# Optimization experiments

Hardware: AMD Instinct MI355X
Metric: run time of the kernel (lower is better)

## Reference

```python
import jax, jax.numpy as jnp
import numpy as np


def _side(x, y, W, w):
    # x: [B, Lx, d] attends over y: [B, Ly, d]
    alpha = jnp.einsum('bld,de->ble', x, W)          # bilinear projection
    alpha = jnp.einsum('ble,bme->blm', alpha, y)     # [B, Lx, Ly]
    alpha = jax.nn.softmax(alpha, axis=1)            # Keras softmax axis=1 (over Lx)
    a = jnp.einsum('blm,bmd->bld', alpha, y)         # attended context [B, Lx, d]
    out = jnp.concatenate([x - a, x * a], axis=-1)   # [B, Lx, 2d]
    beta = jax.nn.softmax(jnp.einsum('ble,eo->blo', out, w)[..., 0], axis=-1)  # [B, Lx]
    return jnp.einsum('bl,ble->be', beta, out)       # pooled [B, 2d]


def setup_inputs() -> dict:
    key = jax.random.key(0)
    k1, k2, k3, k4 = jax.random.split(key, 4)
    B, L, d = 512, 256, 512
    return {
        'i': jax.random.normal(k1, (B, L, d), dtype=jnp.float32),
        'j': jax.random.normal(k2, (B, L, d), dtype=jnp.float32),
        'W': jax.random.normal(k3, (d, d), dtype=jnp.float32) * 0.05,
        'w': jax.random.normal(k4, (2 * d, 1), dtype=jnp.float32) * 0.05,
    }


def reference(i, j, W, w):
    out_i = _side(i, j, W, w)
    out_j = _side(j, i, W, w)
    return (out_i, out_j)
```

## Files before the change

kernel.cpp:

```cpp
#include <hip/hip_runtime.h>

#define LL 256
#define DD 512

typedef _Float16 f16;
typedef _Float16 f16x4_t __attribute__((ext_vector_type(4)));
typedef _Float16 f16x8_t __attribute__((ext_vector_type(8)));
typedef float f32x4_t __attribute__((ext_vector_type(4)));

__device__ __forceinline__ f16x8_t cvt2(const float4 a, const float4 b) {
  f16x8_t v;
  v[0] = (f16)a.x; v[1] = (f16)a.y; v[2] = (f16)a.z; v[3] = (f16)a.w;
  v[4] = (f16)b.x; v[5] = (f16)b.y; v[6] = (f16)b.z; v[7] = (f16)b.w;
  return v;
}

__device__ __forceinline__ void gl16(const void* g, void* l) {
  __builtin_amdgcn_global_load_lds(
      (const __attribute__((address_space(1))) void*)g,
      (__attribute__((address_space(3))) void*)l, 16, 0, 0);
}

__global__ void k_prep(const float* __restrict__ W, f16* __restrict__ Wt) {
  __shared__ float t[64][65];
  int bx = blockIdx.x & 7;
  int by = blockIdx.x >> 3;
  int tx = threadIdx.x & 63, tg = threadIdx.x >> 6;
  for (int r = tg; r < 64; r += 4)
    t[r][tx] = W[(by * 64 + r) * DD + bx * 64 + tx];
  __syncthreads();
  for (int r = tg; r < 64; r += 4)
    Wt[(bx * 64 + r) * DD + by * 64 + tx] = (f16)t[tx][r];
}


__global__ __launch_bounds__(512, 2)
void k_main(const float* __restrict__ gi, const float* __restrict__ gj,
            const f16* __restrict__ Wt, const float* __restrict__ wv,
            f16* __restrict__ slabs, float* __restrict__ out) {
  __shared__ __align__(16) char R1[131072];
  __shared__ __align__(16) char R2[16384];

  const int tid = threadIdx.x;
  const int lane = tid & 63;
  const int wave = tid >> 6;
  const int lq = lane & 15, lg = lane >> 4;

  const int sb = blockIdx.x;
  const int wk = (sb & 7) * 128 + (sb >> 3);
  const int b = wk >> 1, side = wk & 1;
  const float* __restrict__ x = (side ? gj : gi) + (size_t)b * (LL * DD);
  const float* __restrict__ y = (side ? gi : gj) + (size_t)b * (LL * DD);
  f16* __restrict__ slab = slabs + (size_t)wk * (LL * DD);

  char* const R1c = R1;
  char* const R2c = R2;
  float* const colred = (float*)R2c;
  float* const colmax = (float*)(R2c + 2048);
  float* const colinv = (float*)(R2c + 3072);
  float* const gp     = (float*)R2c;
  float* const betas  = (float*)(R2c + 2048);

  {
    const int wl2 = wave & 1, we4 = wave >> 1;
    for (int lh = 0; lh < 2; ++lh) {
      f32x4_t acc[4][8];
#pragma unroll
      for (int lf = 0; lf < 4; ++lf)
#pragma unroll
        for (int ef = 0; ef < 8; ++ef) acc[lf][ef] = (f32x4_t){0.f, 0.f, 0.f, 0.f};

      const int xrow = tid >> 2;
      const int xc4 = (tid & 3) * 16;
      {
        const float* src = x + (size_t)(lh * 128 + xrow) * DD + xc4;
        float4 a0 = *(const float4*)src, a1 = *(const float4*)(src + 4);
        float4 a2 = *(const float4*)(src + 8), a3 = *(const float4*)(src + 12);
        unsigned swz = (unsigned)(xrow & 7) << 4;
        *(f16x8_t*)(R1c + xrow * 128 + ((xc4 * 2) ^ swz)) = cvt2(a0, a1);
        *(f16x8_t*)(R1c + xrow * 128 + ((xc4 * 2 + 16) ^ swz)) = cvt2(a2, a3);
      }
      __syncthreads();

      for (int s = 0; s < 8; ++s) {
        char* xbc = R1c + (s & 1) * 16384;
        char* xbn = R1c + ((s + 1) & 1) * 16384;
        float4 p0, p1, p2, p3;
        if (s < 7) {
          const float* src = x + (size_t)(lh * 128 + xrow) * DD + (s + 1) * 64 + xc4;
          p0 = *(const float4*)src; p1 = *(const float4*)(src + 4);
          p2 = *(const float4*)(src + 8); p3 = *(const float4*)(src + 12);
        }
#pragma unroll
        for (int ks = 0; ks < 2; ++ks) {
          f16x8_t aF[4], bF[8];
#pragma unroll
          for (int lf = 0; lf < 4; ++lf) {
            int row = wl2 * 64 + lf * 16 + lq;
            aF[lf] = *(const f16x8_t*)(xbc + row * 128 +
                       ((ks * 64 + lg * 16) ^ ((unsigned)(row & 7) << 4)));
          }
#pragma unroll
          for (int ef = 0; ef < 8; ++ef) {
            int er = we4 * 128 + ef * 16 + lq;
            bF[ef] = *(const f16x8_t*)(Wt + (size_t)er * DD + s * 64 + ks * 32 + lg * 8);
          }
#pragma unroll
          for (int lf = 0; lf < 4; ++lf)
#pragma unroll
            for (int ef = 0; ef < 8; ++ef)
              acc[lf][ef] = __builtin_amdgcn_mfma_f32_16x16x32_f16(aF[lf], bF[ef], acc[lf][ef], 0, 0, 0);
        }
        if (s < 7) {
          unsigned swz = (unsigned)(xrow & 7) << 4;
          *(f16x8_t*)(xbn + xrow * 128 + ((xc4 * 2) ^ swz)) = cvt2(p0, p1);
          *(f16x8_t*)(xbn + xrow * 128 + ((xc4 * 2 + 16) ^ swz)) = cvt2(p2, p3);
        }
        __syncthreads();
      }
#pragma unroll
      for (int lf = 0; lf < 4; ++lf)
#pragma unroll
        for (int ef = 0; ef < 8; ++ef) {
          int e = we4 * 128 + ef * 16 + lq;
          int l0 = lh * 128 + wl2 * 64 + lf * 16 + lg * 4;
#pragma unroll
          for (int r = 0; r < 4; ++r) {
            int l = l0 + r;
            size_t byte = (size_t)l * 1024 + (size_t)(e >> 6) * 128 +
                          (unsigned)(((e & 63) * 2) ^ ((l & 7) << 4));
            *(f16*)((char*)slab + byte) = (f16)acc[lf][ef][r];
          }
        }
    }
  }
  __threadfence_block();
  __syncthreads();

  {
    const int wm = wave & 3, wl = wave >> 2;
    f32x4_t accS[4][8];
#pragma unroll
    for (int mf = 0; mf < 4; ++mf)
#pragma unroll
      for (int nf = 0; nf < 8; ++nf) accS[mf][nf] = (f32x4_t){0.f, 0.f, 0.f, 0.f};

    const int prow = tid >> 1, phalf = tid & 1;
    const int lsub = lane >> 3, lin8 = lane & 7;

    auto stageBP = [&](int s, int buf) {
#pragma unroll
      for (int q = 0; q < 4; ++q) {
        int lrow = (q * 8 + wave) * 8 + lsub;
        const char* g = (const char*)slab + (size_t)lrow * 1024 + (size_t)s * 128 + lin8 * 16;
        gl16(g, R1c + buf * 32768 + (q * 8 + wave) * 1024);
      }
    };

    stageBP(0, 0);
    {
      unsigned swz = (unsigned)(prow & 7) << 4;
      const float* src = y + (size_t)prow * DD + phalf * 32;
#pragma unroll
      for (int q = 0; q < 4; ++q) {
        float4 a0 = *(const float4*)(src + q * 8);
        float4 a1 = *(const float4*)(src + q * 8 + 4);
        *(f16x8_t*)(R1c + 65536 + prow * 128 + ((phalf * 64 + q * 16) ^ swz)) = cvt2(a0, a1);
      }
    }
    __syncthreads();

    for (int s = 0; s < 8; ++s) {
      const char* BPc = R1c + (s & 1) * 32768;
      const char* Yc = R1c + 65536 + (s & 1) * 32768;
      float4 pre_y[8];
      if (s < 7) {
        stageBP(s + 1, (s + 1) & 1);
        const float* src = y + (size_t)prow * DD + (s + 1) * 64 + phalf * 32;
#pragma unroll
        for (int q = 0; q < 8; ++q) pre_y[q] = *(const float4*)(src + q * 4);
      }
#pragma unroll
      for (int ks = 0; ks < 2; ++ks) {
        f16x8_t aF[4], bF[8];
#pragma unroll
        for (int mf = 0; mf < 4; ++mf) {
          int row = wm * 64 + mf * 16 + lq;
          aF[mf] = *(const f16x8_t*)(Yc + row * 128 +
                     ((ks * 64 + lg * 16) ^ ((unsigned)(row & 7) << 4)));
        }
#pragma unroll
        for (int nf = 0; nf < 8; ++nf) {
          int row = wl * 128 + nf * 16 + lq;
          bF[nf] = *(const f16x8_t*)(BPc + row * 128 +
                     ((ks * 64 + lg * 16) ^ ((unsigned)(row & 7) << 4)));
        }
#pragma unroll
        for (int mf = 0; mf < 4; ++mf)
#pragma unroll
          for (int nf = 0; nf < 8; ++nf)
            accS[mf][nf] = __builtin_amdgcn_mfma_f32_16x16x32_f16(aF[mf], bF[nf], accS[mf][nf], 0, 0, 0);
      }
      if (s < 7) {
        char* Yn = R1c + 65536 + ((s + 1) & 1) * 32768;
        unsigned swz = (unsigned)(prow & 7) << 4;
#pragma unroll
        for (int q = 0; q < 4; ++q)
          *(f16x8_t*)(Yn + prow * 128 + ((phalf * 64 + q * 16) ^ swz)) =
              cvt2(pre_y[2 * q], pre_y[2 * q + 1]);
      }
      __syncthreads();
    }

    float red[4][4];
#pragma unroll
    for (int mf = 0; mf < 4; ++mf)
#pragma unroll
      for (int r = 0; r < 4; ++r) {
        float v = accS[mf][0][r];
#pragma unroll
        for (int nf = 1; nf < 8; ++nf) v = fmaxf(v, accS[mf][nf][r]);
        v = fmaxf(v, __shfl_xor(v, 1));
        v = fmaxf(v, __shfl_xor(v, 2));
        v = fmaxf(v, __shfl_xor(v, 4));
        v = fmaxf(v, __shfl_xor(v, 8));
        red[mf][r] = v;
      }
    if (lq == 0) {
#pragma unroll
      for (int mf = 0; mf < 4; ++mf)
#pragma unroll
        for (int r = 0; r < 4; ++r)
          colred[wl * 256 + wm * 64 + mf * 16 + lg * 4 + r] = red[mf][r];
    }
    __syncthreads();
    if (tid < 256) colmax[tid] = fmaxf(colred[tid], colred[256 + tid]);
    __syncthreads();
    float cm[4][4];
#pragma unroll
    for (int mf = 0; mf < 4; ++mf)
#pragma unroll
      for (int r = 0; r < 4; ++r) cm[mf][r] = colmax[wm * 64 + mf * 16 + lg * 4 + r];
    __syncthreads();
#pragma unroll
    for (int mf = 0; mf < 4; ++mf)
#pragma unroll
      for (int r = 0; r < 4; ++r) {
        float s = 0.f;
#pragma unroll
        for (int nf = 0; nf < 8; ++nf) {
          float p = __expf(accS[mf][nf][r] - cm[mf][r]);
          accS[mf][nf][r] = p;
          s += p;
        }
        s += __shfl_xor(s, 1);
        s += __shfl_xor(s, 2);
        s += __shfl_xor(s, 4);
        s += __shfl_xor(s, 8);
        red[mf][r] = s;
      }
    if (lq == 0) {
#pragma unroll
      for (int mf = 0; mf < 4; ++mf)
#pragma unroll
        for (int r = 0; r < 4; ++r)
          colred[wl * 256 + wm * 64 + mf * 16 + lg * 4 + r] = red[mf][r];
    }
    __syncthreads();
    if (tid < 256) colinv[tid] = 1.f / (colred[tid] + colred[256 + tid]);
    __syncthreads();
    float inv[4][4];
#pragma unroll
    for (int mf = 0; mf < 4; ++mf)
#pragma unroll
      for (int r = 0; r < 4; ++r) inv[mf][r] = colinv[wm * 64 + mf * 16 + lg * 4 + r];
    __syncthreads();
#pragma unroll
    for (int mf = 0; mf < 4; ++mf)
#pragma unroll
      for (int nf = 0; nf < 8; ++nf) {
        int l = wl * 128 + nf * 16 + lq;
        f16x4_t v;
        v[0] = (f16)(accS[mf][nf][0] * inv[mf][0]);
        v[1] = (f16)(accS[mf][nf][1] * inv[mf][1]);
        v[2] = (f16)(accS[mf][nf][2] * inv[mf][2]);
        v[3] = (f16)(accS[mf][nf][3] * inv[mf][3]);
        *(f16x4_t*)(R1c + l * 512 +
                    ((wm * 128 + mf * 32 + lg * 8) ^ ((unsigned)(l & 7) << 4))) = v;
      }
  }
  __syncthreads();

  {
    const int wl3 = wave & 3, wd = wave >> 2;
    float garr[4][4];
#pragma unroll
    for (int lf = 0; lf < 4; ++lf)
#pragma unroll
      for (int r = 0; r < 4; ++r) garr[lf][r] = 0.f;

    const int yd = tid & 127, ymq = tid >> 7;
    f16* const a_ = slab;

    for (int dct = 0; dct < 4; ++dct) {
      f32x4_t accB[4][4];
#pragma unroll
      for (int lf = 0; lf < 4; ++lf)
#pragma unroll
        for (int df = 0; df < 4; ++df) accB[lf][df] = (f32x4_t){0.f, 0.f, 0.f, 0.f};

      float lyA[4][4], lyB[4][4];
#pragma unroll
      for (int q = 0; q < 4; ++q) {
        int m0 = ymq * 16 + q * 4;
#pragma unroll
        for (int k = 0; k < 4; ++k)
          lyA[q][k] = y[(size_t)(m0 + k) * DD + dct * 128 + yd];
      }
#pragma unroll
      for (int mh = 0; mh < 4; ++mh) {
        __syncthreads();
        {
          unsigned swz = (unsigned)(yd & 7) << 4;
#pragma unroll
          for (int q = 0; q < 4; ++q) {
            int m0 = ymq * 16 + q * 4;
            f16x4_t v;
            if (mh & 1) {
              v[0] = (f16)lyB[q][0]; v[1] = (f16)lyB[q][1];
              v[2] = (f16)lyB[q][2]; v[3] = (f16)lyB[q][3];
            } else {
              v[0] = (f16)lyA[q][0]; v[1] = (f16)lyA[q][1];
              v[2] = (f16)lyA[q][2]; v[3] = (f16)lyA[q][3];
            }
            *(f16x4_t*)(R2c + yd * 128 + ((m0 * 2) ^ swz)) = v;
          }
        }
        __syncthreads();
        if (mh < 3) {
#pragma unroll
          for (int q = 0; q < 4; ++q) {
            int m0 = (mh + 1) * 64 + ymq * 16 + q * 4;
#pragma unroll
            for (int k = 0; k < 4; ++k) {
              float lv = y[(size_t)(m0 + k) * DD + dct * 128 + yd];
              if (mh & 1) lyA[q][k] = lv; else lyB[q][k] = lv;
            }
          }
        }
#pragma unroll
        for (int ks = 0; ks < 2; ++ks) {
          f16x8_t aF[4], bF[4];
#pragma unroll
          for (int lf = 0; lf < 4; ++lf) {
            int row = wl3 * 64 + lf * 16 + lq;
            aF[lf] = *(const f16x8_t*)(R1c + row * 512 +
                       ((mh * 128 + ks * 64 + lg * 16) ^ ((unsigned)(row & 7) << 4)));
          }
#pragma unroll
          for (int df = 0; df < 4; ++df) {
            int row = wd * 64 + df * 16 + lq;
            bF[df] = *(const f16x8_t*)(R2c + row * 128 +
                       ((ks * 64 + lg * 16) ^ ((unsigned)(row & 7) << 4)));
          }
#pragma unroll
          for (int lf = 0; lf < 4; ++lf)
#pragma unroll
            for (int df = 0; df < 4; ++df)
              accB[lf][df] = __builtin_amdgcn_mfma_f32_16x16x32_f16(aF[lf], bF[df], accB[lf][df], 0, 0, 0);
        }
      }
      float wvA[4], wvB[4];
#pragma unroll
      for (int df = 0; df < 4; ++df) {
        int d = dct * 128 + wd * 64 + df * 16 + lq;
        wvA[df] = wv[d];
        wvB[df] = wv[DD + d];
      }
#pragma unroll
      for (int lf = 0; lf < 4; ++lf)
#pragma unroll
        for (int r = 0; r < 4; ++r) {
          int l = wl3 * 64 + lf * 16 + lg * 4 + r;
          float gs = 0.f;
#pragma unroll
          for (int df = 0; df < 4; ++df) {
            int d = dct * 128 + wd * 64 + df * 16 + lq;
            float av = accB[lf][df][r];
            float xv = x[(size_t)l * DD + d];
            gs += (xv - av) * wvA[df] + (xv * av) * wvB[df];
            a_[(size_t)l * DD + d] = (f16)av;
          }
          gs += __shfl_xor(gs, 1);
          gs += __shfl_xor(gs, 2);
          gs += __shfl_xor(gs, 4);
          gs += __shfl_xor(gs, 8);
          garr[lf][r] += gs;
        }
    }
    __syncthreads();
    if (lq == 0) {
#pragma unroll
      for (int lf = 0; lf < 4; ++lf)
#pragma unroll
        for (int r = 0; r < 4; ++r)
          gp[wd * 256 + wl3 * 64 + lf * 16 + lg * 4 + r] = garr[lf][r];
    }
  }
  __threadfence_block();
  __syncthreads();

  if (wave == 0) {
    float gv[4];
    float M = -3.4e38f;
#pragma unroll
    for (int q = 0; q < 4; ++q) {
      int l = lane + q * 64;
      gv[q] = gp[l] + gp[256 + l];
      M = fmaxf(M, gv[q]);
    }
#pragma unroll
    for (int s = 1; s < 64; s <<= 1) M = fmaxf(M, __shfl_xor(M, s));
    float S = 0.f, ev[4];
#pragma unroll
    for (int q = 0; q < 4; ++q) { ev[q] = __expf(gv[q] - M); S += ev[q]; }
#pragma unroll
    for (int s = 1; s < 64; s <<= 1) S += __shfl_xor(S, s);
    float inv = 1.f / S;
#pragma unroll
    for (int q = 0; q < 4; ++q) betas[lane + q * 64] = ev[q] * inv;
  }
  __syncthreads();

  {
    const f16* const a_ = slab;
    int dc = tid;
    float s1 = 0.f, s2 = 0.f;
    for (int l = 0; l < 256; ++l) {
      float bl = betas[l];
      float av = (float)a_[(size_t)l * DD + dc];
      float xv = x[(size_t)l * DD + dc];
      s1 += bl * (xv - av);
      s2 += bl * (xv * av);
    }
    size_t o = (size_t)side * (512u * 1024u) + (size_t)b * 1024u;
    out[o + dc] = s1;
    out[o + DD + dc] = s2;
  }
}

extern "C" void kernel_launch(void* const* d_in, const int* in_sizes, int n_in,
                              void* d_out, int out_size, void* d_ws, size_t ws_size,
                              hipStream_t stream) {
  (void)in_sizes; (void)n_in; (void)out_size; (void)ws_size;
  const float* gi = (const float*)d_in[0];
  const float* gj = (const float*)d_in[1];
  const float* W  = (const float*)d_in[2];
  const float* wv = (const float*)d_in[3];
  float* out = (float*)d_out;
  f16* Wt = (f16*)d_ws;
  f16* slabs = Wt + DD * DD;
  k_prep<<<dim3(64), dim3(256), 0, stream>>>(W, Wt);
  k_main<<<dim3(1024), dim3(512), 0, stream>>>(gi, gj, Wt, wv, slabs, out);
}
```

Baseline: 959.5 us.

## Fuse projection into score GEMM, keeping projected tiles in LDS instead of global slab

```diff
diff --git a/kernel.cpp b/kernel.cpp
--- a/kernel.cpp
+++ b/kernel.cpp
@@ -13,12 +13,6 @@
   v[0] = (f16)a.x; v[1] = (f16)a.y; v[2] = (f16)a.z; v[3] = (f16)a.w;
   v[4] = (f16)b.x; v[5] = (f16)b.y; v[6] = (f16)b.z; v[7] = (f16)b.w;
   return v;
-}
-
-__device__ __forceinline__ void gl16(const void* g, void* l) {
-  __builtin_amdgcn_global_load_lds(
-      (const __attribute__((address_space(1))) void*)g,
-      (__attribute__((address_space(3))) void*)l, 16, 0, 0);
 }
 
 __global__ void k_prep(const float* __restrict__ W, f16* __restrict__ Wt) {
@@ -55,242 +49,182 @@
 
   char* const R1c = R1;
   char* const R2c = R2;
-  float* const colred = (float*)R2c;
-  float* const colmax = (float*)(R2c + 2048);
-  float* const colinv = (float*)(R2c + 3072);
-  float* const gp     = (float*)R2c;
-  float* const betas  = (float*)(R2c + 2048);
-
-  {
-    const int wl2 = wave & 1, we4 = wave >> 1;
-    for (int lh = 0; lh < 2; ++lh) {
-      f32x4_t acc[4][8];
-#pragma unroll
-      for (int lf = 0; lf < 4; ++lf)
-#pragma unroll
-        for (int ef = 0; ef < 8; ++ef) acc[lf][ef] = (f32x4_t){0.f, 0.f, 0.f, 0.f};
-
-      const int xrow = tid >> 2;
-      const int xc4 = (tid & 3) * 16;
+
+  f32x4_t accS[2][16];
+#pragma unroll
+  for (int mf = 0; mf < 2; ++mf)
+#pragma unroll
+    for (int nfg = 0; nfg < 16; ++nfg) accS[mf][nfg] = (f32x4_t){0.f, 0.f, 0.f, 0.f};
+
+  const int wvl = wave & 1, wve = wave >> 1;
+  const int xrow = tid >> 3, xsl = tid & 7;
+  const int prow = tid >> 1, phalf = tid & 1;
+
+#pragma unroll
+  for (int q = 0; q < 4; ++q) {
+#pragma unroll
+    for (int eh = 0; eh < 2; ++eh) {
+      f32x4_t acc[4][2];
+#pragma unroll
+      for (int ef = 0; ef < 4; ++ef)
+#pragma unroll
+        for (int lf = 0; lf < 2; ++lf) acc[ef][lf] = (f32x4_t){0.f, 0.f, 0.f, 0.f};
+
       {
-        const float* src = x + (size_t)(lh * 128 + xrow) * DD + xc4;
+        const float* src = x + (size_t)(q * 64 + xrow) * DD + xsl * 8;
         float4 a0 = *(const float4*)src, a1 = *(const float4*)(src + 4);
-        float4 a2 = *(const float4*)(src + 8), a3 = *(const float4*)(src + 12);
-        unsigned swz = (unsigned)(xrow & 7) << 4;
-        *(f16x8_t*)(R1c + xrow * 128 + ((xc4 * 2) ^ swz)) = cvt2(a0, a1);
-        *(f16x8_t*)(R1c + xrow * 128 + ((xc4 * 2 + 16) ^ swz)) = cvt2(a2, a3);
+        *(f16x8_t*)(R2c + xrow * 128 + ((xsl * 16) ^ ((unsigned)(xrow & 7) << 4))) =
+            cvt2(a0, a1);
       }
       __syncthreads();
 
       for (int s = 0; s < 8; ++s) {
-        char* xbc = R1c + (s & 1) * 16384;
-        char* xbn = R1c + ((s + 1) & 1) * 16384;
-        float4 p0, p1, p2, p3;
+        char* xc = R2c + (s & 1) * 8192;
+        char* xn = R2c + ((s + 1) & 1) * 8192;
+        float4 p0, p1;
         if (s < 7) {
-          const float* src = x + (size_t)(lh * 128 + xrow) * DD + (s + 1) * 64 + xc4;
+          const float* src = x + (size_t)(q * 64 + xrow) * DD + (s + 1) * 64 + xsl * 8;
           p0 = *(const float4*)src; p1 = *(const float4*)(src + 4);
-          p2 = *(const float4*)(src + 8); p3 = *(const float4*)(src + 12);
         }
 #pragma unroll
         for (int ks = 0; ks < 2; ++ks) {
-          f16x8_t aF[4], bF[8];
-#pragma unroll
-          for (int lf = 0; lf < 4; ++lf) {
-            int row = wl2 * 64 + lf * 16 + lq;
-            aF[lf] = *(const f16x8_t*)(xbc + row * 128 +
-                       ((ks * 64 + lg * 16) ^ ((unsigned)(row & 7) << 4)));
-          }
-#pragma unroll
-          for (int ef = 0; ef < 8; ++ef) {
-            int er = we4 * 128 + ef * 16 + lq;
-            bF[ef] = *(const f16x8_t*)(Wt + (size_t)er * DD + s * 64 + ks * 32 + lg * 8);
-          }
-#pragma unroll
-          for (int lf = 0; lf < 4; ++lf)
-#pragma unroll
-            for (int ef = 0; ef < 8; ++ef)
-              acc[lf][ef] = __builtin_amdgcn_mfma_f32_16x16x32_f16(aF[lf], bF[ef], acc[lf][ef], 0, 0, 0);
+          f16x8_t aF[4], bF[2];
+#pragma unroll
+          for (int ef = 0; ef < 4; ++ef) {
+            int e = eh * 256 + wve * 64 + ef * 16 + lq;
+            aF[ef] = *(const f16x8_t*)(Wt + (size_t)e * DD + s * 64 + ks * 32 + lg * 8);
+          }
+#pragma unroll
+          for (int lf = 0; lf < 2; ++lf) {
+            int l = wvl * 32 + lf * 16 + lq;
+            bF[lf] = *(const f16x8_t*)(xc + l * 128 +
+                       ((ks * 64 + lg * 16) ^ ((unsigned)(l & 7) << 4)));
+          }
+#pragma unroll
+          for (int ef = 0; ef < 4; ++ef)
+#pragma unroll
+            for (int lf = 0; lf < 2; ++lf)
+              acc[ef][lf] = __builtin_amdgcn_mfma_f32_16x16x32_f16(aF[ef], bF[lf], acc[ef][lf], 0, 0, 0);
         }
         if (s < 7) {
-          unsigned swz = (unsigned)(xrow & 7) << 4;
-          *(f16x8_t*)(xbn + xrow * 128 + ((xc4 * 2) ^ swz)) = cvt2(p0, p1);
-          *(f16x8_t*)(xbn + xrow * 128 + ((xc4 * 2 + 16) ^ swz)) = cvt2(p2, p3);
+          *(f16x8_t*)(xn + xrow * 128 + ((xsl * 16) ^ ((unsigned)(xrow & 7) << 4))) =
+              cvt2(p0, p1);
         }
         __syncthreads();
       }
 #pragma unroll
-      for (int lf = 0; lf < 4; ++lf)
-#pragma unroll
-        for (int ef = 0; ef < 8; ++ef) {
-          int e = we4 * 128 + ef * 16 + lq;
-          int l0 = lh * 128 + wl2 * 64 + lf * 16 + lg * 4;
-#pragma unroll
-          for (int r = 0; r < 4; ++r) {
-            int l = l0 + r;
-            size_t byte = (size_t)l * 1024 + (size_t)(e >> 6) * 128 +
-                          (unsigned)(((e & 63) * 2) ^ ((l & 7) << 4));
-            *(f16*)((char*)slab + byte) = (f16)acc[lf][ef][r];
-          }
-        }
-    }
-  }
-  __threadfence_block();
-  __syncthreads();
-
-  {
-    const int wm = wave & 3, wl = wave >> 2;
-    f32x4_t accS[4][8];
-#pragma unroll
-    for (int mf = 0; mf < 4; ++mf)
-#pragma unroll
-      for (int nf = 0; nf < 8; ++nf) accS[mf][nf] = (f32x4_t){0.f, 0.f, 0.f, 0.f};
-
-    const int prow = tid >> 1, phalf = tid & 1;
-    const int lsub = lane >> 3, lin8 = lane & 7;
-
-    auto stageBP = [&](int s, int buf) {
-#pragma unroll
-      for (int q = 0; q < 4; ++q) {
-        int lrow = (q * 8 + wave) * 8 + lsub;
-        const char* g = (const char*)slab + (size_t)lrow * 1024 + (size_t)s * 128 + lin8 * 16;
-        gl16(g, R1c + buf * 32768 + (q * 8 + wave) * 1024);
-      }
-    };
-
-    stageBP(0, 0);
+      for (int ef = 0; ef < 4; ++ef)
+#pragma unroll
+        for (int lf = 0; lf < 2; ++lf) {
+          int l_loc = wvl * 32 + lf * 16 + lq;
+          int e0 = eh * 256 + wve * 64 + ef * 16 + lg * 4;
+          f16x4_t v;
+          v[0] = (f16)acc[ef][lf][0]; v[1] = (f16)acc[ef][lf][1];
+          v[2] = (f16)acc[ef][lf][2]; v[3] = (f16)acc[ef][lf][3];
+          *(f16x4_t*)(R1c + l_loc * 1024 + (e0 >> 6) * 128 +
+                      (((unsigned)((e0 & 63) * 2)) ^ ((unsigned)(l_loc & 7) << 4))) = v;
+        }
+    }
+    __syncthreads();
+
     {
-      unsigned swz = (unsigned)(prow & 7) << 4;
       const float* src = y + (size_t)prow * DD + phalf * 32;
-#pragma unroll
-      for (int q = 0; q < 4; ++q) {
-        float4 a0 = *(const float4*)(src + q * 8);
-        float4 a1 = *(const float4*)(src + q * 8 + 4);
-        *(f16x8_t*)(R1c + 65536 + prow * 128 + ((phalf * 64 + q * 16) ^ swz)) = cvt2(a0, a1);
+      unsigned bk = (unsigned)(prow & 7) << 4;
+#pragma unroll
+      for (int u = 0; u < 4; ++u) {
+        float4 a0 = *(const float4*)(src + u * 8);
+        float4 a1 = *(const float4*)(src + u * 8 + 4);
+        *(f16x8_t*)(R1c + 65536 + prow * 128 + ((phalf * 64 + u * 16) ^ bk)) = cvt2(a0, a1);
       }
     }
     __syncthreads();
 
     for (int s = 0; s < 8; ++s) {
-      const char* BPc = R1c + (s & 1) * 32768;
       const char* Yc = R1c + 65536 + (s & 1) * 32768;
       float4 pre_y[8];
       if (s < 7) {
-        stageBP(s + 1, (s + 1) & 1);
         const float* src = y + (size_t)prow * DD + (s + 1) * 64 + phalf * 32;
 #pragma unroll
-        for (int q = 0; q < 8; ++q) pre_y[q] = *(const float4*)(src + q * 4);
+        for (int u = 0; u < 8; ++u) pre_y[u] = *(const float4*)(src + u * 4);
       }
 #pragma unroll
       for (int ks = 0; ks < 2; ++ks) {
-        f16x8_t aF[4], bF[8];
-#pragma unroll
-        for (int mf = 0; mf < 4; ++mf) {
-          int row = wm * 64 + mf * 16 + lq;
-          aF[mf] = *(const f16x8_t*)(Yc + row * 128 +
-                     ((ks * 64 + lg * 16) ^ ((unsigned)(row & 7) << 4)));
-        }
-#pragma unroll
-        for (int nf = 0; nf < 8; ++nf) {
-          int row = wl * 128 + nf * 16 + lq;
-          bF[nf] = *(const f16x8_t*)(BPc + row * 128 +
-                     ((ks * 64 + lg * 16) ^ ((unsigned)(row & 7) << 4)));
-        }
-#pragma unroll
-        for (int mf = 0; mf < 4; ++mf)
-#pragma unroll
-          for (int nf = 0; nf < 8; ++nf)
-            accS[mf][nf] = __builtin_amdgcn_mfma_f32_16x16x32_f16(aF[mf], bF[nf], accS[mf][nf], 0, 0, 0);
+        f16x8_t aF[2], bF[4];
+#pragma unroll
+        for (int mf = 0; mf < 2; ++mf) {
+          int m = wave * 32 + mf * 16 + lq;
+          aF[mf] = *(const f16x8_t*)(Yc + m * 128 +
+                     ((ks * 64 + lg * 16) ^ ((unsigned)(m & 7) << 4)));
+        }
+#pragma unroll
+        for (int nf = 0; nf < 4; ++nf) {
+          int l_loc = nf * 16 + lq;
+          bF[nf] = *(const f16x8_t*)(R1c + l_loc * 1024 + s * 128 +
+                     ((ks * 64 + lg * 16) ^ ((unsigned)(l_loc & 7) << 4)));
+        }
+#pragma unroll
+        for (int mf = 0; mf < 2; ++mf)
+#pragma unroll
+          for (int nf = 0; nf < 4; ++nf)
+            accS[mf][q * 4 + nf] =
+                __builtin_amdgcn_mfma_f32_16x16x32_f16(aF[mf], bF[nf], accS[mf][q * 4 + nf], 0, 0, 0);
       }
       if (s < 7) {
         char* Yn = R1c + 65536 + ((s + 1) & 1) * 32768;
-        unsigned swz = (unsigned)(prow & 7) << 4;
-#pragma unroll
-        for (int q = 0; q < 4; ++q)
-          *(f16x8_t*)(Yn + prow * 128 + ((phalf * 64 + q * 16) ^ swz)) =
-              cvt2(pre_y[2 * q], pre_y[2 * q + 1]);
+        unsigned bk = (unsigned)(prow & 7) << 4;
+#pragma unroll
+        for (int u = 0; u < 4; ++u)
+          *(f16x8_t*)(Yn + prow * 128 + ((phalf * 64 + u * 16) ^ bk)) =
+              cvt2(pre_y[2 * u], pre_y[2 * u + 1]);
       }
       __syncthreads();
     }
-
-    float red[4][4];
-#pragma unroll
-    for (int mf = 0; mf < 4; ++mf)
-#pragma unroll
-      for (int r = 0; r < 4; ++r) {
-        float v = accS[mf][0][r];
-#pragma unroll
-        for (int nf = 1; nf < 8; ++nf) v = fmaxf(v, accS[mf][nf][r]);
-        v = fmaxf(v, __shfl_xor(v, 1));
-        v = fmaxf(v, __shfl_xor(v, 2));
-        v = fmaxf(v, __shfl_xor(v, 4));
-        v = fmaxf(v, __shfl_xor(v, 8));
-        red[mf][r] = v;
-      }
-    if (lq == 0) {
-#pragma unroll
-      for (int mf = 0; mf < 4; ++mf)
-#pragma unroll
-        for (int r = 0; r < 4; ++r)
-          colred[wl * 256 + wm * 64 + mf * 16 + lg * 4 + r] = red[mf][r];
-    }
-    __syncthreads();
-    if (tid < 256) colmax[tid] = fmaxf(colred[tid], colred[256 + tid]);
-    __syncthreads();
-    float cm[4][4];
-#pragma unroll
-    for (int mf = 0; mf < 4; ++mf)
-#pragma unroll
-      for (int r = 0; r < 4; ++r) cm[mf][r] = colmax[wm * 64 + mf * 16 + lg * 4 + r];
-    __syncthreads();
-#pragma unroll
-    for (int mf = 0; mf < 4; ++mf)
-#pragma unroll
-      for (int r = 0; r < 4; ++r) {
-        float s = 0.f;
-#pragma unroll
-        for (int nf = 0; nf < 8; ++nf) {
-          float p = __expf(accS[mf][nf][r] - cm[mf][r]);
-          accS[mf][nf][r] = p;
-          s += p;
-        }
-        s += __shfl_xor(s, 1);
-        s += __shfl_xor(s, 2);
-        s += __shfl_xor(s, 4);
-        s += __shfl_xor(s, 8);
-        red[mf][r] = s;
-      }
-    if (lq == 0) {
-#pragma unroll
-      for (int mf = 0; mf < 4; ++mf)
-#pragma unroll
-        for (int r = 0; r < 4; ++r)
-          colred[wl * 256 + wm * 64 + mf * 16 + lg * 4 + r] = red[mf][r];
-    }
-    __syncthreads();
-    if (tid < 256) colinv[tid] = 1.f / (colred[tid] + colred[256 + tid]);
-    __syncthreads();
-    float inv[4][4];
-#pragma unroll
-    for (int mf = 0; mf < 4; ++mf)
-#pragma unroll
-      for (int r = 0; r < 4; ++r) inv[mf][r] = colinv[wm * 64 + mf * 16 + lg * 4 + r];
-    __syncthreads();
-#pragma unroll
-    for (int mf = 0; mf < 4; ++mf)
-#pragma unroll
-      for (int nf = 0; nf < 8; ++nf) {
-        int l = wl * 128 + nf * 16 + lq;
-        f16x4_t v;
-        v[0] = (f16)(accS[mf][nf][0] * inv[mf][0]);
-        v[1] = (f16)(accS[mf][nf][1] * inv[mf][1]);
-        v[2] = (f16)(accS[mf][nf][2] * inv[mf][2]);
-        v[3] = (f16)(accS[mf][nf][3] * inv[mf][3]);
-        *(f16x4_t*)(R1c + l * 512 +
-                    ((wm * 128 + mf * 32 + lg * 8) ^ ((unsigned)(l & 7) << 4))) = v;
-      }
   }
+
+  float inv_[2][4];
+#pragma unroll
+  for (int mf = 0; mf < 2; ++mf)
+#pragma unroll
+    for (int r = 0; r < 4; ++r) {
+      float v = accS[mf][0][r];
+#pragma unroll
+      for (int nfg = 1; nfg < 16; ++nfg) v = fmaxf(v, accS[mf][nfg][r]);
+      v = fmaxf(v, __shfl_xor(v, 1));
+      v = fmaxf(v, __shfl_xor(v, 2));
+      v = fmaxf(v, __shfl_xor(v, 4));
+      v = fmaxf(v, __shfl_xor(v, 8));
+      float ss = 0.f;
+#pragma unroll
+      for (int nfg = 0; nfg < 16; ++nfg) {
+        float p = __expf(accS[mf][nfg][r] - v);
+        accS[mf][nfg][r] = p;
+        ss += p;
+      }
+      ss += __shfl_xor(ss, 1);
+      ss += __shfl_xor(ss, 2);
+      ss += __shfl_xor(ss, 4);
+      ss += __shfl_xor(ss, 8);
+      inv_[mf][r] = 1.f / ss;
+    }
+
+#pragma unroll
+  for (int mf = 0; mf < 2; ++mf)
+#pragma unroll
+    for (int nfg = 0; nfg < 16; ++nfg) {
+      int l = nfg * 16 + lq;
+      int m0 = wave * 32 + mf * 16 + lg * 4;
+      f16x4_t v;
+      v[0] = (f16)(accS[mf][nfg][0] * inv_[mf][0]);
+      v[1] = (f16)(accS[mf][nfg][1] * inv_[mf][1]);
+      v[2] = (f16)(accS[mf][nfg][2] * inv_[mf][2]);
+      v[3] = (f16)(accS[mf][nfg][3] * inv_[mf][3]);
+      *(f16x4_t*)(R1c + l * 512 +
+                  (((unsigned)(m0 * 2)) ^ ((unsigned)(l & 7) << 4))) = v;
+    }
   __syncthreads();
 
+  float* const gp    = (float*)R2c;
+  float* const betas = (float*)(R2c + 2048);
   {
     const int wl3 = wave & 3, wd = wave >> 2;
     float garr[4][4];
@@ -311,11 +245,11 @@
 
       float lyA[4][4], lyB[4][4];
 #pragma unroll
-      for (int q = 0; q < 4; ++q) {
-        int m0 = ymq * 16 + q * 4;
+      for (int u = 0; u < 4; ++u) {
+        int m0 = ymq * 16 + u * 4;
 #pragma unroll
         for (int k = 0; k < 4; ++k)
-          lyA[q][k] = y[(size_t)(m0 + k) * DD + dct * 128 + yd];
+          lyA[u][k] = y[(size_t)(m0 + k) * DD + dct * 128 + yd];
       }
 #pragma unroll
       for (int mh = 0; mh < 4; ++mh) {
@@ -323,15 +257,15 @@
         {
           unsigned swz = (unsigned)(yd & 7) << 4;
 #pragma unroll
-          for (int q = 0; q < 4; ++q) {
-            int m0 = ymq * 16 + q * 4;
+          for (int u = 0; u < 4; ++u) {
+            int m0 = ymq * 16 + u * 4;
             f16x4_t v;
             if (mh & 1) {
-              v[0] = (f16)lyB[q][0]; v[1] = (f16)lyB[q][1];
-              v[2] = (f16)lyB[q][2]; v[3] = (f16)lyB[q][3];
+              v[0] = (f16)lyB[u][0]; v[1] = (f16)lyB[u][1];
+              v[2] = (f16)lyB[u][2]; v[3] = (f16)lyB[u][3];
             } else {
-              v[0] = (f16)lyA[q][0]; v[1] = (f16)lyA[q][1];
-              v[2] = (f16)lyA[q][2]; v[3] = (f16)lyA[q][3];
+              v[0] = (f16)lyA[u][0]; v[1] = (f16)lyA[u][1];
+              v[2] = (f16)lyA[u][2]; v[3] = (f16)lyA[u][3];
             }
             *(f16x4_t*)(R2c + yd * 128 + ((m0 * 2) ^ swz)) = v;
           }
@@ -339,12 +273,12 @@
         __syncthreads();
         if (mh < 3) {
 #pragma unroll
-          for (int q = 0; q < 4; ++q) {
-            int m0 = (mh + 1) * 64 + ymq * 16 + q * 4;
+          for (int u = 0; u < 4; ++u) {
+            int m0 = (mh + 1) * 64 + ymq * 16 + u * 4;
 #pragma unroll
             for (int k = 0; k < 4; ++k) {
               float lv = y[(size_t)(m0 + k) * DD + dct * 128 + yd];
-              if (mh & 1) lyA[q][k] = lv; else lyB[q][k] = lv;
+              if (mh & 1) lyA[u][k] = lv; else lyB[u][k] = lv;
             }
           }
         }
@@ -414,21 +348,21 @@
     float gv[4];
     float M = -3.4e38f;
 #pragma unroll
-    for (int q = 0; q < 4; ++q) {
-      int l = lane + q * 64;
-      gv[q] = gp[l] + gp[256 + l];
-      M = fmaxf(M, gv[q]);
+    for (int u = 0; u < 4; ++u) {
+      int l = lane + u * 64;
+      gv[u] = gp[l] + gp[256 + l];
+      M = fmaxf(M, gv[u]);
     }
 #pragma unroll
     for (int s = 1; s < 64; s <<= 1) M = fmaxf(M, __shfl_xor(M, s));
     float S = 0.f, ev[4];
 #pragma unroll
-    for (int q = 0; q < 4; ++q) { ev[q] = __expf(gv[q] - M); S += ev[q]; }
+    for (int u = 0; u < 4; ++u) { ev[u] = __expf(gv[u] - M); S += ev[u]; }
 #pragma unroll
     for (int s = 1; s < 64; s <<= 1) S += __shfl_xor(S, s);
     float inv = 1.f / S;
 #pragma unroll
-    for (int q = 0; q < 4; ++q) betas[lane + q * 64] = ev[q] * inv;
+    for (int u = 0; u < 4; ++u) betas[lane + u * 64] = ev[u] * inv;
   }
   __syncthreads();
 
```

Measured after the change: 2.379 ms. +148.0%, slower.

## Recompute attended context instead of storing slab, load S-GEMM operands directly from global

Applied to the files above, without the earlier changes.

```diff
diff --git a/kernel.cpp b/kernel.cpp
--- a/kernel.cpp
+++ b/kernel.cpp
@@ -13,12 +13,6 @@
   v[0] = (f16)a.x; v[1] = (f16)a.y; v[2] = (f16)a.z; v[3] = (f16)a.w;
   v[4] = (f16)b.x; v[5] = (f16)b.y; v[6] = (f16)b.z; v[7] = (f16)b.w;
   return v;
-}
-
-__device__ __forceinline__ void gl16(const void* g, void* l) {
-  __builtin_amdgcn_global_load_lds(
-      (const __attribute__((address_space(1))) void*)g,
-      (__attribute__((address_space(3))) void*)l, 16, 0, 0);
 }
 
 __global__ void k_prep(const float* __restrict__ W, f16* __restrict__ Wt) {
@@ -40,6 +34,7 @@
             f16* __restrict__ slabs, float* __restrict__ out) {
   __shared__ __align__(16) char R1[131072];
   __shared__ __align__(16) char R2[16384];
+  __shared__ __align__(16) char R3[8192];
 
   const int tid = threadIdx.x;
   const int lane = tid & 63;
@@ -58,8 +53,10 @@
   float* const colred = (float*)R2c;
   float* const colmax = (float*)(R2c + 2048);
   float* const colinv = (float*)(R2c + 3072);
-  float* const gp     = (float*)R2c;
-  float* const betas  = (float*)(R2c + 2048);
+  float* const gp     = (float*)R3;
+  float* const betas  = (float*)(R3 + 2048);
+  float* const s1dct  = (float*)(R3 + 3072);
+  float* const s2dct  = (float*)(R3 + 5120);
 
   {
     const int wl2 = wave & 1, we4 = wave >> 1;
@@ -145,55 +142,23 @@
 #pragma unroll
       for (int nf = 0; nf < 8; ++nf) accS[mf][nf] = (f32x4_t){0.f, 0.f, 0.f, 0.f};
 
-    const int prow = tid >> 1, phalf = tid & 1;
-    const int lsub = lane >> 3, lin8 = lane & 7;
-
-    auto stageBP = [&](int s, int buf) {
-#pragma unroll
-      for (int q = 0; q < 4; ++q) {
-        int lrow = (q * 8 + wave) * 8 + lsub;
-        const char* g = (const char*)slab + (size_t)lrow * 1024 + (size_t)s * 128 + lin8 * 16;
-        gl16(g, R1c + buf * 32768 + (q * 8 + wave) * 1024);
-      }
-    };
-
-    stageBP(0, 0);
-    {
-      unsigned swz = (unsigned)(prow & 7) << 4;
-      const float* src = y + (size_t)prow * DD + phalf * 32;
-#pragma unroll
-      for (int q = 0; q < 4; ++q) {
-        float4 a0 = *(const float4*)(src + q * 8);
-        float4 a1 = *(const float4*)(src + q * 8 + 4);
-        *(f16x8_t*)(R1c + 65536 + prow * 128 + ((phalf * 64 + q * 16) ^ swz)) = cvt2(a0, a1);
-      }
-    }
-    __syncthreads();
-
+#pragma unroll 2
     for (int s = 0; s < 8; ++s) {
-      const char* BPc = R1c + (s & 1) * 32768;
-      const char* Yc = R1c + 65536 + (s & 1) * 32768;
-      float4 pre_y[8];
-      if (s < 7) {
-        stageBP(s + 1, (s + 1) & 1);
-        const float* src = y + (size_t)prow * DD + (s + 1) * 64 + phalf * 32;
-#pragma unroll
-        for (int q = 0; q < 8; ++q) pre_y[q] = *(const float4*)(src + q * 4);
-      }
 #pragma unroll
       for (int ks = 0; ks < 2; ++ks) {
         f16x8_t aF[4], bF[8];
 #pragma unroll
         for (int mf = 0; mf < 4; ++mf) {
-          int row = wm * 64 + mf * 16 + lq;
-          aF[mf] = *(const f16x8_t*)(Yc + row * 128 +
-                     ((ks * 64 + lg * 16) ^ ((unsigned)(row & 7) << 4)));
+          int m = wm * 64 + mf * 16 + lq;
+          const float* src = y + (size_t)m * DD + s * 64 + ks * 32 + lg * 8;
+          float4 a0 = *(const float4*)src, a1 = *(const float4*)(src + 4);
+          aF[mf] = cvt2(a0, a1);
         }
 #pragma unroll
         for (int nf = 0; nf < 8; ++nf) {
-          int row = wl * 128 + nf * 16 + lq;
-          bF[nf] = *(const f16x8_t*)(BPc + row * 128 +
-                     ((ks * 64 + lg * 16) ^ ((unsigned)(row & 7) << 4)));
+          int l = wl * 128 + nf * 16 + lq;
+          bF[nf] = *(const f16x8_t*)((const char*)slab + (size_t)l * 1024 + s * 128 +
+                     ((ks * 64 + lg * 16) ^ ((unsigned)(l & 7) << 4)));
         }
 #pragma unroll
         for (int mf = 0; mf < 4; ++mf)
@@ -201,15 +166,6 @@
           for (int nf = 0; nf < 8; ++nf)
             accS[mf][nf] = __builtin_amdgcn_mfma_f32_16x16x32_f16(aF[mf], bF[nf], accS[mf][nf], 0, 0, 0);
       }
-      if (s < 7) {
-        char* Yn = R1c + 65536 + ((s + 1) & 1) * 32768;
-        unsigned swz = (unsigned)(prow & 7) << 4;
-#pragma unroll
-        for (int q = 0; q < 4; ++q)
-          *(f16x8_t*)(Yn + prow * 128 + ((phalf * 64 + q * 16) ^ swz)) =
-              cvt2(pre_y[2 * q], pre_y[2 * q + 1]);
-      }
-      __syncthreads();
     }
 
     float red[4][4];
@@ -291,16 +247,79 @@
   }
   __syncthreads();
 
+  const int wl3 = wave & 3, wd = wave >> 2;
+  const int yd = tid & 127, ymq = tid >> 7;
+
+  auto run_dct = [&](int dct, f32x4_t (&accB)[4][4]) {
+    float lyA[4][4], lyB[4][4];
+#pragma unroll
+    for (int u = 0; u < 4; ++u) {
+      int m0 = ymq * 16 + u * 4;
+#pragma unroll
+      for (int k = 0; k < 4; ++k)
+        lyA[u][k] = y[(size_t)(m0 + k) * DD + dct * 128 + yd];
+    }
+#pragma unroll
+    for (int mh = 0; mh < 4; ++mh) {
+      __syncthreads();
+      {
+        unsigned swz = (unsigned)(yd & 7) << 4;
+#pragma unroll
+        for (int u = 0; u < 4; ++u) {
+          int m0 = ymq * 16 + u * 4;
+          f16x4_t v;
+          if (mh & 1) {
+            v[0] = (f16)lyB[u][0]; v[1] = (f16)lyB[u][1];
+            v[2] = (f16)lyB[u][2]; v[3] = (f16)lyB[u][3];
+          } else {
+            v[0] = (f16)lyA[u][0]; v[1] = (f16)lyA[u][1];
+            v[2] = (f16)lyA[u][2]; v[3] = (f16)lyA[u][3];
+          }
+          *(f16x4_t*)(R2c + yd * 128 + ((m0 * 2) ^ swz)) = v;
+        }
+      }
+      __syncthreads();
+      if (mh < 3) {
+#pragma unroll
+        for (int u = 0; u < 4; ++u) {
+          int m0 = (mh + 1) * 64 + ymq * 16 + u * 4;
+#pragma unroll
+          for (int k = 0; k < 4; ++k) {
+            float lv = y[(size_t)(m0 + k) * DD + dct * 128 + yd];
+            if (mh & 1) lyA[u][k] = lv; else lyB[u][k] = lv;
+          }
+        }
+      }
+#pragma unroll
+      for (int ks = 0; ks < 2; ++ks) {
+        f16x8_t aF[4], bF[4];
+#pragma unroll
+        for (int lf = 0; lf < 4; ++lf) {
+          int row = wl3 * 64 + lf * 16 + lq;
+          aF[lf] = *(const f16x8_t*)(R1c + row * 512 +
+                     ((mh * 128 + ks * 64 + lg * 16) ^ ((unsigned)(row & 7) << 4)));
+        }
+#pragma unroll
+        for (int df = 0; df < 4; ++df) {
+          int row = wd * 64 + df * 16 + lq;
+          bF[df] = *(const f16x8_t*)(R2c + row * 128 +
+                     ((ks * 64 + lg * 16) ^ ((unsigned)(row & 7) << 4)));
+        }
+#pragma unroll
+        for (int lf = 0; lf < 4; ++lf)
+#pragma unroll
+          for (int df = 0; df < 4; ++df)
+            accB[lf][df] = __builtin_amdgcn_mfma_f32_16x16x32_f16(aF[lf], bF[df], accB[lf][df], 0, 0, 0);
+      }
+    }
+  };
+
   {
-    const int wl3 = wave & 3, wd = wave >> 2;
     float garr[4][4];
 #pragma unroll
     for (int lf = 0; lf < 4; ++lf)
 #pragma unroll
       for (int r = 0; r < 4; ++r) garr[lf][r] = 0.f;
-
-    const int yd = tid & 127, ymq = tid >> 7;
-    f16* const a_ = slab;
 
     for (int dct = 0; dct < 4; ++dct) {
       f32x4_t accB[4][4];
@@ -308,68 +327,8 @@
       for (int lf = 0; lf < 4; ++lf)
 #pragma unroll
         for (int df = 0; df < 4; ++df) accB[lf][df] = (f32x4_t){0.f, 0.f, 0.f, 0.f};
-
-      float lyA[4][4], lyB[4][4];
-#pragma unroll
-      for (int q = 0; q < 4; ++q) {
-        int m0 = ymq * 16 + q * 4;
-#pragma unroll
-        for (int k = 0; k < 4; ++k)
-          lyA[q][k] = y[(size_t)(m0 + k) * DD + dct * 128 + yd];
-      }
-#pragma unroll
-      for (int mh = 0; mh < 4; ++mh) {
-        __syncthreads();
-        {
-          unsigned swz = (unsigned)(yd & 7) << 4;
-#pragma unroll
-          for (int q = 0; q < 4; ++q) {
-            int m0 = ymq * 16 + q * 4;
-            f16x4_t v;
-            if (mh & 1) {
-              v[0] = (f16)lyB[q][0]; v[1] = (f16)lyB[q][1];
-              v[2] = (f16)lyB[q][2]; v[3] = (f16)lyB[q][3];
-            } else {
-              v[0] = (f16)lyA[q][0]; v[1] = (f16)lyA[q][1];
-              v[2] = (f16)lyA[q][2]; v[3] = (f16)lyA[q][3];
-            }
-            *(f16x4_t*)(R2c + yd * 128 + ((m0 * 2) ^ swz)) = v;
-          }
-        }
-        __syncthreads();
-        if (mh < 3) {
-#pragma unroll
-          for (int q = 0; q < 4; ++q) {
-            int m0 = (mh + 1) * 64 + ymq * 16 + q * 4;
-#pragma unroll
-            for (int k = 0; k < 4; ++k) {
-              float lv = y[(size_t)(m0 + k) * DD + dct * 128 + yd];
-              if (mh & 1) lyA[q][k] = lv; else lyB[q][k] = lv;
-            }
-          }
-        }
-#pragma unroll
-        for (int ks = 0; ks < 2; ++ks) {
-          f16x8_t aF[4], bF[4];
-#pragma unroll
-          for (int lf = 0; lf < 4; ++lf) {
-            int row = wl3 * 64 + lf * 16 + lq;
-            aF[lf] = *(const f16x8_t*)(R1c + row * 512 +
-                       ((mh * 128 + ks * 64 + lg * 16) ^ ((unsigned)(row & 7) << 4)));
-          }
-#pragma unroll
-          for (int df = 0; df < 4; ++df) {
-            int row = wd * 64 + df * 16 + lq;
-            bF[df] = *(const f16x8_t*)(R2c + row * 128 +
-                       ((ks * 64 + lg * 16) ^ ((unsigned)(row & 7) << 4)));
-          }
-#pragma unroll
-          for (int lf = 0; lf < 4; ++lf)
-#pragma unroll
-            for (int df = 0; df < 4; ++df)
-              accB[lf][df] = __builtin_amdgcn_mfma_f32_16x16x32_f16(aF[lf], bF[df], accB[lf][df], 0, 0, 0);
-        }
-      }
+      run_dct(dct, accB);
+
       float wvA[4], wvB[4];
 #pragma unroll
       for (int df = 0; df < 4; ++df) {
@@ -389,7 +348,6 @@
             float av = accB[lf][df][r];
             float xv = x[(size_t)l * DD + d];
             gs += (xv - av) * wvA[df] + (xv * av) * wvB[df];
-            a_[(size_t)l * DD + d] = (f16)av;
           }
           gs += __shfl_xor(gs, 1);
           gs += __shfl_xor(gs, 2);
@@ -407,45 +365,87 @@
           gp[wd * 256 + wl3 * 64 + lf * 16 + lg * 4 + r] = garr[lf][r];
     }
   }
-  __threadfence_block();
   __syncthreads();
 
   if (wave == 0) {
     float gv[4];
     float M = -3.4e38f;
 #pragma unroll
-    for (int q = 0; q < 4; ++q) {
-      int l = lane + q * 64;
-      gv[q] = gp[l] + gp[256 + l];
-      M = fmaxf(M, gv[q]);
+    for (int u = 0; u < 4; ++u) {
+      int l = lane + u * 64;
+      gv[u] = gp[l] + gp[256 + l];
+      M = fmaxf(M, gv[u]);
     }
 #pragma unroll
     for (int s = 1; s < 64; s <<= 1) M = fmaxf(M, __shfl_xor(M, s));
     float S = 0.f, ev[4];
 #pragma unroll
-    for (int q = 0; q < 4; ++q) { ev[q] = __expf(gv[q] - M); S += ev[q]; }
+    for (int u = 0; u < 4; ++u) { ev[u] = __expf(gv[u] - M); S += ev[u]; }
 #pragma unroll
     for (int s = 1; s < 64; s <<= 1) S += __shfl_xor(S, s);
     float inv = 1.f / S;
 #pragma unroll
-    for (int q = 0; q < 4; ++q) betas[lane + q * 64] = ev[q] * inv;
+    for (int u = 0; u < 4; ++u) betas[lane + u * 64] = ev[u] * inv;
   }
   __syncthreads();
 
   {
-    const f16* const a_ = slab;
-    int dc = tid;
-    float s1 = 0.f, s2 = 0.f;
-    for (int l = 0; l < 256; ++l) {
-      float bl = betas[l];
-      float av = (float)a_[(size_t)l * DD + dc];
-      float xv = x[(size_t)l * DD + dc];
-      s1 += bl * (xv - av);
-      s2 += bl * (xv * av);
-    }
-    size_t o = (size_t)side * (512u * 1024u) + (size_t)b * 1024u;
-    out[o + dc] = s1;
-    out[o + DD + dc] = s2;
+    float bl_[4][4];
+#pragma unroll
+    for (int lf = 0; lf < 4; ++lf)
+#pragma unroll
+      for (int r = 0; r < 4; ++r)
+        bl_[lf][r] = betas[wl3 * 64 + lf * 16 + lg * 4 + r];
+
+    for (int dct = 0; dct < 4; ++dct) {
+      f32x4_t accB[4][4];
+#pragma unroll
+      for (int lf = 0; lf < 4; ++lf)
+#pragma unroll
+        for (int df = 0; df < 4; ++df) accB[lf][df] = (f32x4_t){0.f, 0.f, 0.f, 0.f};
+      run_dct(dct, accB);
+
+      float s1p[4] = {0.f, 0.f, 0.f, 0.f};
+      float s2p[4] = {0.f, 0.f, 0.f, 0.f};
+#pragma unroll
+      for (int lf = 0; lf < 4; ++lf)
+#pragma unroll
+        for (int r = 0; r < 4; ++r) {
+          int l = wl3 * 64 + lf * 16 + lg * 4 + r;
+          float bl = bl_[lf][r];
+#pragma unroll
+          for (int df = 0; df < 4; ++df) {
+            int d = dct * 128 + wd * 64 + df * 16 + lq;
+            float av = accB[lf][df][r];
+            float xv = x[(size_t)l * DD + d];
+            s1p[df] += bl * (xv - av);
+            s2p[df] += bl * (xv * av);
+          }
+        }
+#pragma unroll
+      for (int df = 0; df < 4; ++df) {
+        s1p[df] += __shfl_xor(s1p[df], 16);
+        s1p[df] += __shfl_xor(s1p[df], 32);
+        s2p[df] += __shfl_xor(s2p[df], 16);
+        s2p[df] += __shfl_xor(s2p[df], 32);
+      }
+      if (lg == 0) {
+#pragma unroll
+        for (int df = 0; df < 4; ++df) {
+          int dl = wd * 64 + df * 16 + lq;
+          s1dct[wl3 * 128 + dl] = s1p[df];
+          s2dct[wl3 * 128 + dl] = s2p[df];
+        }
+      }
+      __syncthreads();
+      if (tid < 128) {
+        float v1 = s1dct[tid] + s1dct[128 + tid] + s1dct[256 + tid] + s1dct[384 + tid];
+        float v2 = s2dct[tid] + s2dct[128 + tid] + s2dct[256 + tid] + s2dct[384 + tid];
+        size_t o = (size_t)side * (512u * 1024u) + (size_t)b * 1024u;
+        out[o + dct * 128 + tid] = v1;
+        out[o + 512 + dct * 128 + tid] = v2;
+      }
+    }
   }
 }
 
```

New measurement: 1.047 ms. 9.2% more time.
